# Performance work log

Measured on AMD Instinct MI355X. Metric: run time of the kernel, lower is better.

Reference implementation:

```python
import jax, jax.numpy as jnp
import numpy as np

T, B, DG, DH, S = 24, 128, 256, 512, 3
LAM, ETA, EPS_A = 0.95, 0.5, 1e-6   # lambda_decay, eta, epsilon (A-update)
LN_EPS = 1e-5                        # torch LayerNorm default eps
EPS_N = 1e-6                         # norm clamp in inner loop


def setup_inputs() -> dict:
    key = jax.random.key(0)
    ks = jax.random.split(key, 3)
    return {
        "z_seq": jax.random.normal(ks[0], (T, B, DG), jnp.float32),
        "W_h": jax.random.normal(ks[1], (DH, DH), jnp.float32) * (2.0 / DH) ** 0.5,  # kaiming-ish
        "W_g": jax.random.normal(ks[2], (DH, DG), jnp.float32) * (1.0 / DG) ** 0.5,  # xavier-ish
        "b_h": jnp.zeros((DH,), jnp.float32),
        "gamma": jnp.ones((DH,), jnp.float32),
        "beta": jnp.zeros((DH,), jnp.float32),
        "alpha_fw": jnp.ones((1,), jnp.float32),
    }


def _layernorm(x, g, b):
    m = jnp.mean(x, -1, keepdims=True)
    v = jnp.mean((x - m) ** 2, -1, keepdims=True)
    return (x - m) * jax.lax.rsqrt(v + LN_EPS) * g + b


def _compute_k(a):
    k_pos = 1.0 + jax.nn.softplus(a)
    k_neg = 1.0 / (1.0 + jax.nn.softplus(-a))
    return jnp.where(a >= 0, k_pos, k_neg)


def reference(z_seq, W_h, W_g, b_h, gamma, beta, alpha_fw):
    k = _compute_k(alpha_fw[0])

    def step(carry, inp):
        h, A = carry            # h: [B, DH], A: [B, DH, DH]
        z_t, upd = inp          # z_t: [B, DG], upd: scalar bool (t < T-1)
        h_base = h @ W_h.T + z_t @ W_g.T + b_h
        h_s = jax.nn.relu(h_base)
        for _ in range(S):      # inner associative-memory iteration
            Ah = jnp.einsum('bij,bj->bi', A, h_s)
            dot = jnp.sum(h_s * Ah, -1, keepdims=True)
            n1 = jnp.maximum(jnp.linalg.norm(h_s, axis=-1, keepdims=True), EPS_N)
            n2 = jnp.maximum(jnp.linalg.norm(Ah, axis=-1, keepdims=True), EPS_N)
            R_pos = jnp.clip(dot / (n1 * n2), 0.0, 1.0)
            alpha_dyn = 1.0 - (1.0 - R_pos) ** k
            h_s = jax.nn.relu(_layernorm((1.0 - alpha_dyn ** 2) * h_base + alpha_dyn * Ah, gamma, beta))
        # fast-weight Hebbian update (skipped at the last timestep)
        hn2 = jnp.sum(h_s ** 2, -1, keepdims=True) + EPS_A            # [B, 1]
        delta = h_s[:, :, None] * h_s[:, None, :] / hn2[:, :, None]   # [B, DH, DH]
        A_new = jnp.where(upd, LAM * A + ETA * delta, A)
        return (h_s, A_new), None

    h0 = jnp.zeros((B, DH), z_seq.dtype)
    A0 = jnp.zeros((B, DH, DH), z_seq.dtype)
    upd = jnp.arange(T) < (T - 1)
    (h, A), _ = jax.lax.scan(step, (h0, A0), (z_seq, upd))
    return h
```

## Files before the change

### kernel.cpp

```cpp
#include <hip/hip_runtime.h>
#include <hip/hip_fp16.h>
#include <math.h>

#define T_STEPS 24
#define BATCH   128
#define DGI     256
#define DHI     512
#define S_ITERS 3
#define LAMBDA  0.95f
#define ETA     0.5f
#define EPS_A   1e-6f
#define LN_EPS  1e-5f
#define EPS_N   1e-6f
#define HIST_MAX 23
#define NG4      6

static __device__ __forceinline__ float dot2(unsigned int a, unsigned int b, float c) {
#if __has_builtin(__builtin_amdgcn_fdot2)
    typedef _Float16 h2v __attribute__((ext_vector_type(2)));
    return __builtin_amdgcn_fdot2(__builtin_bit_cast(h2v, a),
                                  __builtin_bit_cast(h2v, b), c, false);
#else
    const __half2 ha = __builtin_bit_cast(__half2, a);
    const __half2 hb = __builtin_bit_cast(__half2, b);
    const float2 fa = __half22float2(ha);
    const float2 fb = __half22float2(hb);
    return fmaf(fa.x, fb.x, fmaf(fa.y, fb.y, c));
#endif
}

static __device__ __forceinline__ unsigned int rdlane_u(unsigned int v, int l) {
#if __has_builtin(__builtin_amdgcn_readlane)
    return __builtin_amdgcn_readlane(v, l);
#else
    return __shfl((int)v, l, 64);
#endif
}
static __device__ __forceinline__ float rdlane_f(float v, int l) {
    return __uint_as_float(rdlane_u(__float_as_uint(v), l));
}

static __device__ __forceinline__ float wsum(float v) {
    #pragma unroll
    for (int off = 32; off > 0; off >>= 1) v += __shfl_xor(v, off, 64);
    return v;
}
static __device__ __forceinline__ float dot8(float4 a, float4 b, float4 c, float4 d) {
    float r = a.x * c.x;
    r = fmaf(a.y, c.y, r); r = fmaf(a.z, c.z, r); r = fmaf(a.w, c.w, r);
    r = fmaf(b.x, d.x, r); r = fmaf(b.y, d.y, r); r = fmaf(b.z, d.z, r);
    r = fmaf(b.w, d.w, r);
    return r;
}
static __device__ __forceinline__ float sum8(float4 a, float4 b) {
    return ((a.x + a.y) + (a.z + a.w)) + ((b.x + b.y) + (b.z + b.w));
}

__global__ __launch_bounds__(512)
void prep_k(const float* __restrict__ Wh, unsigned int* __restrict__ P,
            const float* __restrict__ Wg, float* __restrict__ WgT) {
    __shared__ float tile[32][33];
    const int blk = blockIdx.x;
    if (blk < 256) {
        const int j2 = blk;
        const int i  = threadIdx.x;
        const float2 w = *(const float2*)(Wh + (size_t)i * DHI + 2 * j2);
        const __half2 h = __floats2half2_rn(w.x, w.y);
        P[(size_t)j2 * DHI + i] = __builtin_bit_cast(unsigned int, h);
    } else {
        const int tb = blk - 256;
        const int c0 = (tb & 7) * 32;
        const int r0 = (tb >> 3) * 32;
        const int tx = threadIdx.x & 31;
        const int ty = (threadIdx.x >> 5) & 7;
        const bool act = threadIdx.x < 256;
        if (act) {
            #pragma unroll
            for (int i = 0; i < 32; i += 8)
                tile[ty + i][tx] = Wg[(size_t)(r0 + ty + i) * DGI + (c0 + tx)];
        }
        __syncthreads();
        if (act) {
            #pragma unroll
            for (int i = 0; i < 32; i += 8)
                WgT[(size_t)(c0 + ty + i) * DHI + (r0 + tx)] = tile[tx][ty + i];
        }
    }
}

__global__ __launch_bounds__(512)
void zproj_k(const float* __restrict__ z_seq, const float* __restrict__ WgT,
             float* __restrict__ zp) {
    __shared__ __align__(16) float  sh_z[8][DGI];
    __shared__ __align__(16) float4 sh_acc[8][4][128];
    const int b    = blockIdx.x;
    const int t0   = blockIdx.y * 8;
    const int tid  = threadIdx.x;
    const int lane = tid & 63;
    const int wave = tid >> 6;
    {
        const float4* src =
            (const float4*)(z_seq + ((size_t)(t0 + wave) * BATCH + b) * DGI);
        ((float4*)sh_z[wave])[lane] = src[lane];
    }
    __syncthreads();

    const int i4  = tid & 127;
    const int jg  = tid >> 7;
    const int jlo = jg * 64;
    float zreg[8];
    #pragma unroll
    for (int tt = 0; tt < 8; ++tt) zreg[tt] = sh_z[tt][jlo + lane];

    float4 acc[8];
    #pragma unroll
    for (int tt = 0; tt < 8; ++tt) acc[tt] = make_float4(0.f, 0.f, 0.f, 0.f);

    const float4* w4 = (const float4*)WgT;
    #pragma unroll 4
    for (int jj = 0; jj < 64; ++jj) {
        const float4 wv = w4[(size_t)(jlo + jj) * 128 + i4];
        #pragma unroll
        for (int tt = 0; tt < 8; ++tt) {
            const float zv = rdlane_f(zreg[tt], jj);
            acc[tt].x = fmaf(wv.x, zv, acc[tt].x);
            acc[tt].y = fmaf(wv.y, zv, acc[tt].y);
            acc[tt].z = fmaf(wv.z, zv, acc[tt].z);
            acc[tt].w = fmaf(wv.w, zv, acc[tt].w);
        }
    }
    #pragma unroll
    for (int tt = 0; tt < 8; ++tt) sh_acc[tt][jg][i4] = acc[tt];
    __syncthreads();

    const float* af = (const float*)sh_acc;
    #pragma unroll
    for (int tt = 0; tt < 8; ++tt) {
        const int o = tt * 4 * 512;
        const float v = (af[o + tid] + af[o + 512 + tid]) +
                        (af[o + 1024 + tid] + af[o + 1536 + tid]);
        zp[((size_t)b * T_STEPS + t0 + tt) * DHI + tid] = v;
    }
}

__global__ __launch_bounds__(512)
void rnn_v4(const float* __restrict__ zp,
            const unsigned int* __restrict__ P,
            const float* __restrict__ b_h,
            const float* __restrict__ gamma,
            const float* __restrict__ beta,
            const float* __restrict__ alpha_fw,
            float* __restrict__ out) {
    __shared__ __align__(16) float  sh_hist[HIST_MAX][DHI];
    __shared__ __align__(16) float4 sh_hT4[NG4][DHI];
    __shared__ __align__(16) float4 sh_G4[NG4][64];
    __shared__ __align__(16) float  sh_hs[2][DHI];
    __shared__ __align__(16) float  sh_hb[DHI];
    __shared__ __align__(16) float4 sh_part[4][128];
    __shared__ __align__(16) unsigned int sh_h2[DHI / 2];
    __shared__ __align__(16) float  sh_coef[32];
    __shared__ __align__(16) float  sh_dot[32];
    __shared__ __align__(16) float  sh_dhb[32];
    __shared__ __align__(16) float  sh_rsum[32];
    __shared__ float sh_misc[2];

    const int tid  = threadIdx.x;
    const int lane = tid & 63;
    const int wave = tid >> 6;
    const int b    = blockIdx.x;

    const float bh_r = b_h[tid];
    const float g_r  = gamma[tid];
    const float bt_r = beta[tid];

    float kpow;
    {
        const float a  = alpha_fw[0];
        const float ax = fabsf(a);
        const float sp = (ax > 20.f) ? ax : log1pf(expf(ax));
        kpow = (a >= 0.f) ? (1.f + sp) : (1.f / (1.f + sp));
    }

    const int i4  = tid & 127;
    const int jg  = tid >> 7;
    const uint4* __restrict__ wp = (const uint4*)P;
    const int wbase = (jg << 6) * 128 + i4;
    uint4 Wpre[32];
    #pragma unroll
    for (int k = 0; k < 32; ++k) Wpre[k] = wp[wbase + k * 128];

    {
        const float4 z4 = make_float4(0.f, 0.f, 0.f, 0.f);
        for (int i = tid; i < NG4 * DHI; i += DHI) ((float4*)sh_hT4)[i] = z4;
        if (tid < NG4 * 64) ((float4*)sh_G4)[tid] = z4;
        if (tid < 32) { sh_coef[tid] = 0.f; sh_dot[tid] = 0.f;
                        sh_dhb[tid]  = 0.f; sh_rsum[tid] = 0.f; }
        if (tid < 2) sh_misc[tid] = 0.f;
    }
    __syncthreads();

    int   p = 0;
    float hs_i = 0.f, hbase_i = 0.f;
    const size_t zbase = (size_t)b * T_STEPS * DHI + tid;
    float zv = zp[zbase];

    for (int t = 0; t < T_STEPS; ++t) {
        if (t > 0) {
            const unsigned int hreg = sh_h2[(jg << 6) | lane];
            float4 acc = make_float4(0.f, 0.f, 0.f, 0.f);
            uint4 cbuf[2][4];
            #pragma unroll
            for (int k = 0; k < 4; ++k) cbuf[0][k] = wp[wbase + (32 + k) * 128];
            #pragma unroll
            for (int jj = 0; jj < 32; ++jj) {
                const unsigned int hh = rdlane_u(hreg, jj);
                const uint4 wv = Wpre[jj];
                acc.x = dot2(wv.x, hh, acc.x);
                acc.y = dot2(wv.y, hh, acc.y);
                acc.z = dot2(wv.z, hh, acc.z);
                acc.w = dot2(wv.w, hh, acc.w);
            }
            #pragma unroll
            for (int ch = 0; ch < 8; ++ch) {
                if (ch < 7) {
                    #pragma unroll
                    for (int k = 0; k < 4; ++k)
                        cbuf[(ch + 1) & 1][k] = wp[wbase + (36 + ch * 4 + k) * 128];
                }
                #pragma unroll
                for (int k = 0; k < 4; ++k) {
                    const int jj = 32 + ch * 4 + k;
                    const unsigned int hh = rdlane_u(hreg, jj);
                    const uint4 wv = cbuf[ch & 1][k];
                    acc.x = dot2(wv.x, hh, acc.x);
                    acc.y = dot2(wv.y, hh, acc.y);
                    acc.z = dot2(wv.z, hh, acc.z);
                    acc.w = dot2(wv.w, hh, acc.w);
                }
            }
            sh_part[jg][i4] = acc;
            __syncthreads();
            const float* pp = (const float*)sh_part;
            hbase_i = bh_r + zv +
                      ((pp[tid] + pp[512 + tid]) + (pp[1024 + tid] + pp[1536 + tid]));
        } else {
            hbase_i = bh_r + zv;
        }
        sh_hb[tid] = hbase_i;
        hs_i = fmaxf(hbase_i, 0.f);
        p ^= 1;
        sh_hs[p][tid] = hs_i;
        __syncthreads();

        if (t + 1 < T_STEPS) zv = zp[zbase + (size_t)(t + 1) * DHI];

        const int niter = (t == 0) ? 1 : S_ITERS;
        for (int it = 0; it < niter; ++it) {
            {
                const float4* h4p = (const float4*)sh_hs[p];
                const float4 ha = h4p[lane], hc = h4p[64 + lane];
                float4 ba, bc;
                if (it == 0) {
                    const float4* b4p = (const float4*)sh_hb;
                    ba = b4p[lane]; bc = b4p[64 + lane];
                }
                for (int s = wave; s <= t; s += 8) {
                    if (s == t) {
                        float d = dot8(ha, hc, ha, hc);
                        if (it == 0) {
                            float s1 = sum8(ba, bc);
                            float s2 = dot8(ba, bc, ba, bc);
                            d = wsum(d); s1 = wsum(s1); s2 = wsum(s2);
                            if (lane == 0) { sh_dot[t] = d;
                                             sh_misc[0] = s1; sh_misc[1] = s2; }
                        } else {
                            d = wsum(d);
                            if (lane == 0) sh_dot[t] = d;
                        }
                    } else {
                        const float4* v4 = (const float4*)sh_hist[s];
                        const float4 va = v4[lane], vc = v4[64 + lane];
                        float d = dot8(va, vc, ha, hc);
                        if (it == 0) {
                            float e = dot8(va, vc, ba, bc);
                            d = wsum(d); e = wsum(e);
                            if (lane == 0) { sh_dot[s] = d; sh_dhb[s] = e; }
                        } else {
                            d = wsum(d);
                            if (lane == 0) sh_dot[s] = d;
                        }
                    }
                }
            }
            __syncthreads();

            float pa = 0.f, SA = 0.f, SHA = 0.f, gsum = 0.f, Ah = 0.f;
            {
                const float4* c4 = (const float4*)sh_coef;
                const float4* d4 = (const float4*)sh_dot;
                const float4* e4 = (const float4*)sh_dhb;
                const float4* r4 = (const float4*)sh_rsum;
                const int ng = (t + 4) >> 2;
                for (int g = 0; g < ng; ++g) {
                    const float4 cc = c4[g], dd = d4[g], ee = e4[g], rr = r4[g];
                    const float4 gg = sh_G4[g][lane];
                    const float4 hv = sh_hT4[g][tid];
                    const float w0 = cc.x * dd.x, w1 = cc.y * dd.y;
                    const float w2 = cc.z * dd.z, w3 = cc.w * dd.w;
                    pa   = fmaf(w0, dd.x, fmaf(w1, dd.y, fmaf(w2, dd.z, fmaf(w3, dd.w, pa))));
                    SA   = fmaf(w0, rr.x, fmaf(w1, rr.y, fmaf(w2, rr.z, fmaf(w3, rr.w, SA))));
                    SHA  = fmaf(w0, ee.x, fmaf(w1, ee.y, fmaf(w2, ee.z, fmaf(w3, ee.w, SHA))));
                    gsum = fmaf(w0, gg.x, fmaf(w1, gg.y, fmaf(w2, gg.z, fmaf(w3, gg.w, gsum))));
                    Ah   = fmaf(w0, hv.x, fmaf(w1, hv.y, fmaf(w2, hv.z, fmaf(w3, hv.w, Ah))));
                }
            }
            const float wl = (lane < 32) ? sh_coef[lane] * sh_dot[lane] : 0.f;
            const float pb = wsum(wl * gsum);

            const float n1 = fmaxf(sqrtf(sh_dot[t]), EPS_N);
            const float n2 = fmaxf(sqrtf(fmaxf(pb, 0.f)), EPS_N);
            float R = pa / (n1 * n2);
            R = fminf(fmaxf(R, 0.f), 1.f);
            const float alpha = 1.f - __powf(1.f - R, kpow);
            const float c = 1.f - alpha * alpha;

            const float S1 = sh_misc[0], S2 = sh_misc[1];
            const float mean = (c * S1 + alpha * SA) * (1.f / DHI);
            float var = (c * c * S2 + 2.f * c * alpha * SHA + alpha * alpha * pb)
                        * (1.f / DHI) - mean * mean;
            var = fmaxf(var, 0.f);
            const float rstd = rsqrtf(var + LN_EPS);

            const float y = fmaf(c, hbase_i, alpha * Ah);
            hs_i = fmaxf(fmaf((y - mean) * rstd, g_r, bt_r), 0.f);
            p ^= 1;
            sh_hs[p][tid] = hs_i;
            if (it == niter - 1 && t + 1 < T_STEPS) {
                const float partner = __shfl_xor(hs_i, 1);
                if (!(tid & 1)) {
                    const __half2 h2 = __floats2half2_rn(hs_i, partner);
                    sh_h2[tid >> 1] = __builtin_bit_cast(unsigned int, h2);
                }
            }
            __syncthreads();
        }

        if (t < T_STEPS - 1) {
            const float4* h4p = (const float4*)sh_hs[p];
            const float4 ha = h4p[lane], hc = h4p[64 + lane];
            for (int s = wave; s <= t; s += 8) {
                if (s == t) {
                    float d  = dot8(ha, hc, ha, hc);
                    float rs = sum8(ha, hc);
                    d = wsum(d); rs = wsum(rs);
                    if (lane == 0) {
                        ((float*)&sh_G4[t >> 2][t])[t & 3] = d;
                        sh_coef[t] = ETA / (d + EPS_A);
                        sh_rsum[t] = rs;
                    }
                } else {
                    const float4* v4 = (const float4*)sh_hist[s];
                    const float4 va = v4[lane], vc = v4[64 + lane];
                    float d = dot8(va, vc, ha, hc);
                    d = wsum(d);
                    if (lane == 0) {
                        ((float*)&sh_G4[t >> 2][s])[t & 3] = d;
                        ((float*)&sh_G4[s >> 2][t])[s & 3] = d;
                    }
                }
            }
            if (tid < t) sh_coef[tid] *= LAMBDA;
            sh_hist[t][tid] = hs_i;
            ((float*)&sh_hT4[t >> 2][tid])[t & 3] = hs_i;
        } else {
            out[(size_t)b * DHI + tid] = hs_i;
        }
    }
}

__global__ __launch_bounds__(512)
void corernn_fb(const float* __restrict__ z_seq, const float* __restrict__ Wh,
                const float* __restrict__ Wg, const float* __restrict__ b_h,
                const float* __restrict__ gamma, const float* __restrict__ beta,
                const float* __restrict__ alpha_fw, float* __restrict__ out) {
    __shared__ __align__(16) float sh_hist[HIST_MAX][DHI];
    __shared__ __align__(16) float sh_hs[2][DHI];
    __shared__ __align__(16) float sh_G[HIST_MAX][64];
    __shared__ float  sh_coef[32];
    __shared__ float  sh_dot[32];
    __shared__ float2 sh_red[8];
    __shared__ __align__(16) float sh_z[DGI];

    const int tid  = threadIdx.x;
    const int lane = tid & 63;
    const int wave = tid >> 6;
    const int b    = blockIdx.x;
    const float bh_r = b_h[tid];
    const float g_r  = gamma[tid];
    const float bt_r = beta[tid];
    float kpow;
    {
        const float a  = alpha_fw[0];
        const float ax = fabsf(a);
        const float sp = (ax > 20.f) ? ax : log1pf(expf(ax));
        kpow = (a >= 0.f) ? (1.f + sp) : (1.f / (1.f + sp));
    }
    for (int i = tid; i < HIST_MAX * 64; i += DHI) ((float*)sh_G)[i] = 0.f;
    if (tid < DGI) sh_z[tid] = z_seq[(size_t)b * DGI + tid];
    __syncthreads();

    int p = 0;
    float hs_i = 0.f, hbase_i = 0.f;
    for (int t = 0; t < T_STEPS; ++t) {
        float a0 = bh_r, a1 = 0.f, a2 = 0.f, a3 = 0.f;
        {
            const float4* wrow = (const float4*)(Wg + (size_t)tid * DGI);
            const float4* z4   = (const float4*)sh_z;
            #pragma unroll 4
            for (int j4 = 0; j4 < DGI / 4; ++j4) {
                const float4 w = wrow[j4]; const float4 h = z4[j4];
                a0 = fmaf(w.x, h.x, a0); a1 = fmaf(w.y, h.y, a1);
                a2 = fmaf(w.z, h.z, a2); a3 = fmaf(w.w, h.w, a3);
            }
        }
        if (t > 0) {
            const float4* wrow = (const float4*)(Wh + (size_t)tid * DHI);
            const float4* h4   = (const float4*)sh_hs[p];
            #pragma unroll 4
            for (int j4 = 0; j4 < DHI / 4; ++j4) {
                const float4 w = wrow[j4]; const float4 h = h4[j4];
                a0 = fmaf(w.x, h.x, a0); a1 = fmaf(w.y, h.y, a1);
                a2 = fmaf(w.z, h.z, a2); a3 = fmaf(w.w, h.w, a3);
            }
        }
        hbase_i = (a0 + a1) + (a2 + a3);
        hs_i = fmaxf(hbase_i, 0.f);
        p ^= 1; sh_hs[p][tid] = hs_i;
        __syncthreads();

        const int niter = (t == 0) ? 1 : S_ITERS;
        for (int it = 0; it < niter; ++it) {
            const float* hcur = sh_hs[p];
            float h8[8];
            #pragma unroll
            for (int q = 0; q < 8; ++q) h8[q] = hcur[lane + 64 * q];
            for (int s = wave; s <= t; s += 8) {
                float d = 0.f;
                if (s == t) {
                    #pragma unroll
                    for (int q = 0; q < 8; ++q) d = fmaf(h8[q], h8[q], d);
                } else {
                    const float* vr = sh_hist[s];
                    #pragma unroll
                    for (int q = 0; q < 8; ++q) d = fmaf(vr[lane + 64 * q], h8[q], d);
                }
                #pragma unroll
                for (int off = 32; off > 0; off >>= 1) d += __shfl_xor(d, off, 64);
                if (lane == 0) sh_dot[s] = d;
            }
            __syncthreads();
            float dl = 0.f, w_l = 0.f;
            if (lane < t) { dl = sh_dot[lane]; w_l = sh_coef[lane] * dl; }
            float gsum = 0.f, Ah = 0.f;
            for (int s = 0; s < t; ++s) {
                const float ws = sh_coef[s] * sh_dot[s];
                gsum = fmaf(ws, sh_G[s][lane], gsum);
                Ah   = fmaf(ws, sh_hist[s][tid], Ah);
            }
            float pa = w_l * dl, pb = w_l * gsum;
            #pragma unroll
            for (int off = 32; off > 0; off >>= 1) {
                pa += __shfl_xor(pa, off, 64);
                pb += __shfl_xor(pb, off, 64);
            }
            const float n1 = fmaxf(sqrtf(sh_dot[t]), EPS_N);
            const float n2 = fmaxf(sqrtf(fmaxf(pb, 0.f)), EPS_N);
            float R = fminf(fmaxf(pa / (n1 * n2), 0.f), 1.f);
            const float alpha = 1.f - __powf(1.f - R, kpow);
            const float y = (1.f - alpha * alpha) * hbase_i + alpha * Ah;
            float q0 = y, q1 = y * y;
            #pragma unroll
            for (int off = 32; off > 0; off >>= 1) {
                q0 += __shfl_xor(q0, off, 64);
                q1 += __shfl_xor(q1, off, 64);
            }
            if (lane == 0) sh_red[wave] = make_float2(q0, q1);
            __syncthreads();
            float s0 = 0.f, s1 = 0.f;
            #pragma unroll
            for (int w = 0; w < 8; ++w) { const float2 r = sh_red[w]; s0 += r.x; s1 += r.y; }
            const float mean = s0 * (1.f / DHI);
            const float var  = fmaf(s1, 1.f / DHI, -mean * mean);
            const float rstd = rsqrtf(var + LN_EPS);
            hs_i = fmaxf(fmaf((y - mean) * rstd, g_r, bt_r), 0.f);
            p ^= 1; sh_hs[p][tid] = hs_i;
            if (it == niter - 1 && t + 1 < T_STEPS && tid < DGI)
                sh_z[tid] = z_seq[((size_t)(t + 1) * BATCH + b) * DGI + tid];
            __syncthreads();
        }

        if (t < T_STEPS - 1) {
            const float* hcur = sh_hs[p];
            float h8[8];
            #pragma unroll
            for (int q = 0; q < 8; ++q) h8[q] = hcur[lane + 64 * q];
            for (int s = wave; s <= t; s += 8) {
                float d = 0.f;
                if (s == t) {
                    #pragma unroll
                    for (int q = 0; q < 8; ++q) d = fmaf(h8[q], h8[q], d);
                } else {
                    const float* vr = sh_hist[s];
                    #pragma unroll
                    for (int q = 0; q < 8; ++q) d = fmaf(vr[lane + 64 * q], h8[q], d);
                }
                #pragma unroll
                for (int off = 32; off > 0; off >>= 1) d += __shfl_xor(d, off, 64);
                if (lane == 0) {
                    if (s == t) { sh_G[t][t] = d; sh_coef[t] = ETA / (d + EPS_A); }
                    else        { sh_G[t][s] = d; sh_G[s][t] = d; }
                }
            }
            if (tid < t) sh_coef[tid] *= LAMBDA;
            sh_hist[t][tid] = hs_i;
        } else {
            out[(size_t)b * DHI + tid] = hs_i;
        }
    }
}

extern "C" void kernel_launch(void* const* d_in, const int* in_sizes, int n_in,
                              void* d_out, int out_size, void* d_ws, size_t ws_size,
                              hipStream_t stream) {
    const float* z_seq    = (const float*)d_in[0];
    const float* W_h      = (const float*)d_in[1];
    const float* W_g      = (const float*)d_in[2];
    const float* b_h      = (const float*)d_in[3];
    const float* gamma    = (const float*)d_in[4];
    const float* beta     = (const float*)d_in[5];
    const float* alpha_fw = (const float*)d_in[6];
    float* out = (float*)d_out;

    const size_t zp_elems  = (size_t)BATCH * T_STEPS * DHI;
    const size_t wgt_elems = (size_t)DGI * DHI;
    const size_t p_elems   = (size_t)(DHI / 2) * DHI;
    const size_t needed = (zp_elems + wgt_elems) * sizeof(float)
                        + p_elems * sizeof(unsigned int);
    if (ws_size >= needed) {
        float* zp  = (float*)d_ws;
        float* WgT = zp + zp_elems;
        unsigned int* P = (unsigned int*)(WgT + wgt_elems);
        prep_k<<<384, 512, 0, stream>>>(W_h, P, W_g, WgT);
        zproj_k<<<dim3(BATCH, T_STEPS / 8), 512, 0, stream>>>(z_seq, WgT, zp);
        rnn_v4<<<BATCH, 512, 0, stream>>>(zp, P, b_h, gamma, beta, alpha_fw, out);
    } else {
        corernn_fb<<<BATCH, 512, 0, stream>>>(z_seq, W_h, W_g, b_h, gamma, beta,
                                              alpha_fw, out);
    }
}
```

Measured before the change: 378.5 us.

## Fuse z-projection into recurrent kernel and reduce pinned W_h registers

Removes the separate zproj kernel launch and computes the z_seq @ W_g^T projection for all 24 timesteps inside the recurrent kernel. z_seq is staged transposed in the history shared buffer before that buffer is needed for history. Pinned W_h register slices drop from 32 to 24, with the remainder streamed from global memory each step, and launch bounds now request 2 blocks per CU to cap register use. This saves a launch and a global round trip, at the cost of serial per-block projection work, more global W_h reads per step and possible register pressure from the 24 accumulators.

```diff
diff --git a/kernel.cpp b/kernel.cpp
--- a/kernel.cpp
+++ b/kernel.cpp
@@ -14,6 +14,7 @@
 #define EPS_N   1e-6f
 #define HIST_MAX 23
 #define NG4      6
+#define NPIN     24
 
 static __device__ __forceinline__ float dot2(unsigned int a, unsigned int b, float c) {
 #if __has_builtin(__builtin_amdgcn_fdot2)
@@ -35,9 +36,6 @@
 #else
     return __shfl((int)v, l, 64);
 #endif
-}
-static __device__ __forceinline__ float rdlane_f(float v, int l) {
-    return __uint_as_float(rdlane_u(__float_as_uint(v), l));
 }
 
 static __device__ __forceinline__ float wsum(float v) {
@@ -88,63 +86,10 @@
     }
 }
 
-__global__ __launch_bounds__(512)
-void zproj_k(const float* __restrict__ z_seq, const float* __restrict__ WgT,
-             float* __restrict__ zp) {
-    __shared__ __align__(16) float  sh_z[8][DGI];
-    __shared__ __align__(16) float4 sh_acc[8][4][128];
-    const int b    = blockIdx.x;
-    const int t0   = blockIdx.y * 8;
-    const int tid  = threadIdx.x;
-    const int lane = tid & 63;
-    const int wave = tid >> 6;
-    {
-        const float4* src =
-            (const float4*)(z_seq + ((size_t)(t0 + wave) * BATCH + b) * DGI);
-        ((float4*)sh_z[wave])[lane] = src[lane];
-    }
-    __syncthreads();
-
-    const int i4  = tid & 127;
-    const int jg  = tid >> 7;
-    const int jlo = jg * 64;
-    float zreg[8];
-    #pragma unroll
-    for (int tt = 0; tt < 8; ++tt) zreg[tt] = sh_z[tt][jlo + lane];
-
-    float4 acc[8];
-    #pragma unroll
-    for (int tt = 0; tt < 8; ++tt) acc[tt] = make_float4(0.f, 0.f, 0.f, 0.f);
-
-    const float4* w4 = (const float4*)WgT;
-    #pragma unroll 4
-    for (int jj = 0; jj < 64; ++jj) {
-        const float4 wv = w4[(size_t)(jlo + jj) * 128 + i4];
-        #pragma unroll
-        for (int tt = 0; tt < 8; ++tt) {
-            const float zv = rdlane_f(zreg[tt], jj);
-            acc[tt].x = fmaf(wv.x, zv, acc[tt].x);
-            acc[tt].y = fmaf(wv.y, zv, acc[tt].y);
-            acc[tt].z = fmaf(wv.z, zv, acc[tt].z);
-            acc[tt].w = fmaf(wv.w, zv, acc[tt].w);
-        }
-    }
-    #pragma unroll
-    for (int tt = 0; tt < 8; ++tt) sh_acc[tt][jg][i4] = acc[tt];
-    __syncthreads();
-
-    const float* af = (const float*)sh_acc;
-    #pragma unroll
-    for (int tt = 0; tt < 8; ++tt) {
-        const int o = tt * 4 * 512;
-        const float v = (af[o + tid] + af[o + 512 + tid]) +
-                        (af[o + 1024 + tid] + af[o + 1536 + tid]);
-        zp[((size_t)b * T_STEPS + t0 + tt) * DHI + tid] = v;
-    }
-}
-
-__global__ __launch_bounds__(512)
-void rnn_v4(const float* __restrict__ zp,
+__global__ __launch_bounds__(512, 2)
+void rnn_v5(const float* __restrict__ z_seq,
+            float* __restrict__ zp,
+            const float* __restrict__ WgT,
             const unsigned int* __restrict__ P,
             const float* __restrict__ b_h,
             const float* __restrict__ gamma,
@@ -181,14 +126,6 @@
         kpow = (a >= 0.f) ? (1.f + sp) : (1.f / (1.f + sp));
     }
 
-    const int i4  = tid & 127;
-    const int jg  = tid >> 7;
-    const uint4* __restrict__ wp = (const uint4*)P;
-    const int wbase = (jg << 6) * 128 + i4;
-    uint4 Wpre[32];
-    #pragma unroll
-    for (int k = 0; k < 32; ++k) Wpre[k] = wp[wbase + k * 128];
-
     {
         const float4 z4 = make_float4(0.f, 0.f, 0.f, 0.f);
         for (int i = tid; i < NG4 * DHI; i += DHI) ((float4*)sh_hT4)[i] = z4;
@@ -196,23 +133,57 @@
         if (tid < 32) { sh_coef[tid] = 0.f; sh_dot[tid] = 0.f;
                         sh_dhb[tid]  = 0.f; sh_rsum[tid] = 0.f; }
         if (tid < 2) sh_misc[tid] = 0.f;
+        float* shz = (float*)sh_hist;
+        for (int idx = tid; idx < T_STEPS * DGI; idx += DHI) {
+            const int t = idx >> 8, j = idx & 255;
+            shz[j * 28 + t] = z_seq[((size_t)t * BATCH + b) * DGI + j];
+        }
     }
     __syncthreads();
+
+    float zv;
+    {
+        float zacc[T_STEPS];
+        #pragma unroll
+        for (int k = 0; k < T_STEPS; ++k) zacc[k] = 0.f;
+        const float* shz = (const float*)sh_hist;
+        #pragma unroll 4
+        for (int j = 0; j < DGI; ++j) {
+            const float w = WgT[(size_t)j * DHI + tid];
+            const float4* zt4 = (const float4*)(shz + j * 28);
+            #pragma unroll
+            for (int g = 0; g < 6; ++g) {
+                const float4 zq = zt4[g];
+                zacc[4 * g + 0] = fmaf(w, zq.x, zacc[4 * g + 0]);
+                zacc[4 * g + 1] = fmaf(w, zq.y, zacc[4 * g + 1]);
+                zacc[4 * g + 2] = fmaf(w, zq.z, zacc[4 * g + 2]);
+                zacc[4 * g + 3] = fmaf(w, zq.w, zacc[4 * g + 3]);
+            }
+        }
+        #pragma unroll
+        for (int k = 0; k < T_STEPS; ++k)
+            zp[((size_t)b * T_STEPS + k) * DHI + tid] = zacc[k];
+        zv = zacc[0];
+    }
+
+    const int i4 = tid & 127;
+    const int jg = tid >> 7;
+    const uint4* __restrict__ wp = (const uint4*)P;
+    const int wbase = (jg << 6) * 128 + i4;
+    uint4 Wpre[NPIN];
+    #pragma unroll
+    for (int k = 0; k < NPIN; ++k) Wpre[k] = wp[wbase + k * 128];
 
     int   p = 0;
     float hs_i = 0.f, hbase_i = 0.f;
     const size_t zbase = (size_t)b * T_STEPS * DHI + tid;
-    float zv = zp[zbase];
 
     for (int t = 0; t < T_STEPS; ++t) {
         if (t > 0) {
             const unsigned int hreg = sh_h2[(jg << 6) | lane];
             float4 acc = make_float4(0.f, 0.f, 0.f, 0.f);
-            uint4 cbuf[2][4];
-            #pragma unroll
-            for (int k = 0; k < 4; ++k) cbuf[0][k] = wp[wbase + (32 + k) * 128];
-            #pragma unroll
-            for (int jj = 0; jj < 32; ++jj) {
+            #pragma unroll
+            for (int jj = 0; jj < NPIN; ++jj) {
                 const unsigned int hh = rdlane_u(hreg, jj);
                 const uint4 wv = Wpre[jj];
                 acc.x = dot2(wv.x, hh, acc.x);
@@ -220,23 +191,14 @@
                 acc.z = dot2(wv.z, hh, acc.z);
                 acc.w = dot2(wv.w, hh, acc.w);
             }
-            #pragma unroll
-            for (int ch = 0; ch < 8; ++ch) {
-                if (ch < 7) {
-                    #pragma unroll
-                    for (int k = 0; k < 4; ++k)
-                        cbuf[(ch + 1) & 1][k] = wp[wbase + (36 + ch * 4 + k) * 128];
-                }
-                #pragma unroll
-                for (int k = 0; k < 4; ++k) {
-                    const int jj = 32 + ch * 4 + k;
-                    const unsigned int hh = rdlane_u(hreg, jj);
-                    const uint4 wv = cbuf[ch & 1][k];
-                    acc.x = dot2(wv.x, hh, acc.x);
-                    acc.y = dot2(wv.y, hh, acc.y);
-                    acc.z = dot2(wv.z, hh, acc.z);
-                    acc.w = dot2(wv.w, hh, acc.w);
-                }
+            #pragma unroll 8
+            for (int jj = NPIN; jj < 64; ++jj) {
+                const unsigned int hh = rdlane_u(hreg, jj);
+                const uint4 wv = wp[wbase + jj * 128];
+                acc.x = dot2(wv.x, hh, acc.x);
+                acc.y = dot2(wv.y, hh, acc.y);
+                acc.z = dot2(wv.z, hh, acc.z);
+                acc.w = dot2(wv.w, hh, acc.w);
             }
             sh_part[jg][i4] = acc;
             __syncthreads();
@@ -551,8 +513,8 @@
         float* WgT = zp + zp_elems;
         unsigned int* P = (unsigned int*)(WgT + wgt_elems);
         prep_k<<<384, 512, 0, stream>>>(W_h, P, W_g, WgT);
-        zproj_k<<<dim3(BATCH, T_STEPS / 8), 512, 0, stream>>>(z_seq, WgT, zp);
-        rnn_v4<<<BATCH, 512, 0, stream>>>(zp, P, b_h, gamma, beta, alpha_fw, out);
+        rnn_v5<<<BATCH, 512, 0, stream>>>(z_seq, zp, WgT, P, b_h, gamma, beta,
+                                          alpha_fw, out);
     } else {
         corernn_fb<<<BATCH, 512, 0, stream>>>(z_seq, W_h, W_g, b_h, gamma, beta,
                                               alpha_fw, out);
```

Result: faster. 354.2 us (-6.4%).
